# Performance work log

Hardware: AMD Instinct MI355X
Metric: run time of the kernel (lower is better)

Reference implementation:

```python
import jax, jax.numpy as jnp
import numpy as np

# ---- Clifford algebra Cl(4,1) setup -------------------------------------
SIG = [1, 1, 1, 1, -1]
GA = 1 << len(SIG)  # 32
B, S, E, H = 2, 512, 256, 8
HD = E // H


def _cayley_sign(sig):
    """sign[a,b] such that e_a * e_b = sign[a,b] * e_(a XOR b)."""
    n = len(sig)
    G = 1 << n
    M = np.zeros((G, G), np.float32)
    for a in range(G):
        for b in range(G):
            # canonical reordering sign
            ss = 0
            aa = a >> 1
            while aa:
                ss += bin(aa & b).count('1')
                aa >>= 1
            s = -1.0 if (ss & 1) else 1.0
            # metric contraction on shared basis vectors
            common = a & b
            for i in range(n):
                if (common >> i) & 1:
                    s *= sig[i]
            M[a, b] = s
    return M

SIGN = _cayley_sign(SIG)          # [GA, GA]
SIG_DIAG = np.diag(SIGN).copy()   # blade square signs (metric diagonal)


def _manifold_norm(x):
    # normalize each multivector over its GA components
    return x / jnp.sqrt(jnp.sum(x * x, axis=-1, keepdims=True) + 1e-6)


def _geo_linear(x, w):
    """Clifford linear layer: out[...,o,l] = sum_{i,m,n: m^n=l} w[o,i,m] x[...,i,n] sign(m,n).
    x: [B,S,In,GA], w: [Out,In,GA]. Loop over 32 fixed blades (signed permutation + GEMM)."""
    G = x.shape[-1]
    out = 0.0
    for m in range(G):
        perm = np.arange(G) ^ m              # n = m ^ l
        coeff = jnp.asarray(SIGN[m, perm])   # sign(m, n)
        xs = x[..., perm] * coeff            # [B,S,In,GA]
        out = out + jnp.einsum('oi,bsil->bsol', w[:, :, m], xs)
    return out


def _versor_linear(x, w):
    return _manifold_norm(_geo_linear(x, w))


def _forward(x, mask, wq, wk, wv, wo, gamma):
    b, s = x.shape[0], x.shape[1]
    q = _versor_linear(x, wq).reshape(b, s, H, HD, GA).transpose(0, 2, 1, 3, 4)
    k = _versor_linear(x, wk).reshape(b, s, H, HD, GA).transpose(0, 2, 1, 3, 4)
    v = _versor_linear(x, wv).reshape(b, s, H, HD, GA).transpose(0, 2, 1, 3, 4)
    q_flat = q.reshape(b * H, s, HD, GA)
    k_flat = k.reshape(b * H, s, HD, GA)
    sig_diag = jnp.asarray(SIG_DIAG)
    q_sig = q_flat * sig_diag                      # metric-weighted query
    scalar_score = jnp.einsum('bidl,bjdl->bij', q_sig, k_flat)   # [BH,S,S]
    q_norm_sq = jnp.sum(q_flat ** 2, axis=(-1, -2))[:, :, None]  # [BH,S,1]
    k_norm_sq = jnp.sum(k_flat ** 2, axis=(-1, -2))[:, None, :]  # [BH,1,S]
    bivector_norm = jnp.sqrt(jax.nn.relu(q_norm_sq * k_norm_sq - scalar_score ** 2) + 1e-6)
    score = (scalar_score + gamma * bivector_norm) / np.float32(np.sqrt(HD))
    # triangle update (seq > 1)
    score = score + 0.1 * jnp.matmul(jax.nn.softmax(score, axis=-1), score)
    score = score.reshape(b, H, s, s)
    score = jnp.where(mask[:, None, None, :] == 0, jnp.float32(-1e9), score)
    attn_probs = jax.nn.softmax(score, axis=-1)
    out = jnp.einsum('bhij,bhjdl->bhidl', attn_probs, v)
    out = out.transpose(0, 2, 1, 3, 4).reshape(b, s, E, GA)
    return _versor_linear(out, wo)


def setup_inputs() -> dict:
    key = jax.random.key(0)
    ks = jax.random.split(key, 6)
    std = np.float32((2.0 / (E * GA)) ** 0.5)
    x = jax.random.normal(ks[0], (B, S, E, GA), dtype=jnp.float32)
    wq = jax.random.normal(ks[1], (E, E, GA), dtype=jnp.float32) * std
    wk = jax.random.normal(ks[2], (E, E, GA), dtype=jnp.float32) * std
    wv = jax.random.normal(ks[3], (E, E, GA), dtype=jnp.float32) * std
    wo = jax.random.normal(ks[4], (E, E, GA), dtype=jnp.float32) * std
    gamma = jnp.asarray(0.1, dtype=jnp.float32)
    mask = jnp.ones((B, S), dtype=jnp.int32)
    return {'x': x, 'wq': wq, 'wk': wk, 'wv': wv, 'wo': wo, 'gamma': gamma, 'mask': mask}


def reference(x, wq, wk, wv, wo, gamma, mask):
    return _forward(x, mask, wq, wk, wv, wo, gamma)
```

## Files before the change

kernel.cpp:

```cpp
#include <hip/hip_runtime.h>
#include <stdint.h>

typedef unsigned short u16;
typedef unsigned int u32;
typedef __attribute__((ext_vector_type(8))) __bf16 bf16x8;
typedef __attribute__((ext_vector_type(4))) float f32x4;

#define DEVINL __device__ __forceinline__

DEVINL float bf2f(u16 u){ union{u32 i; float f;} c; c.i = ((u32)u)<<16; return c.f; }
DEVINL u16 f2bf(float f){ union{float f; u32 i;} c; c.f=f; u32 u=c.i; return (u16)((u + 0x7fffu + ((u>>16)&1u))>>16); }
DEVINL u32 pack2(float a, float b){ return (u32)f2bf(a) | ((u32)f2bf(b)<<16); }

DEVINL int sign_neg(int a, int b){
  int s = __popc((a>>1)&b) + __popc((a>>2)&b) + __popc((a>>3)&b) + __popc((a>>4)&b) + ((a&b)>>4);
  return s & 1;
}

struct GTab { int col[32][4]; int ph[32][4]; };
constexpr GTab make_gtab(){
  GTab g{};
  int gc[5][4] = {}; int gp[5][4] = {};
  for (int r=0;r<4;r++){
    const int a=(r>>1)&1, b=r&1;
    gc[0][r]=r^2; gp[0][r]=0;
    gc[1][r]=r^2; gp[1][r]= a?1:3;
    gc[2][r]=r^1; gp[2][r]= a?2:0;
    gc[3][r]=r^1; gp[3][r]=((a?2:0)+(b?1:3))&3;
    gc[4][r]=r;   gp[4][r]=(3+(a?2:0)+(b?2:0))&3;
  }
  for (int I=0;I<32;I++){
    for (int r=0;r<4;r++){ g.col[I][r]=r; g.ph[I][r]=0; }
    for (int bit=0;bit<5;bit++) if ((I>>bit)&1){
      for (int r=0;r<4;r++){
        const int c = g.col[I][r];
        g.ph[I][r]  = (g.ph[I][r] + gp[bit][c]) & 3;
        g.col[I][r] = gc[bit][c];
      }
    }
  }
  return g;
}
constexpr GTab GT = make_gtab();

DEVINL void mv2mat(const float (&x)[32], float (&Mre)[4][4], float (&Mim)[4][4]){
  #pragma unroll
  for (int r=0;r<4;r++)
    #pragma unroll
    for (int c=0;c<4;c++){ Mre[r][c]=0.f; Mim[r][c]=0.f; }
  #pragma unroll
  for (int l=0;l<32;l++){
    #pragma unroll
    for (int r=0;r<4;r++){
      constexpr const GTab& G = GT;
      const int c = G.col[l][r], p = G.ph[l][r];
      if (p==0) Mre[r][c] += x[l];
      else if (p==1) Mim[r][c] += x[l];
      else if (p==2) Mre[r][c] -= x[l];
      else Mim[r][c] -= x[l];
    }
  }
}

DEVINL void mat2mv(const float (&v)[4][8], float (&x)[32]){
  #pragma unroll
  for (int l=0;l<32;l++){
    float s = 0.f;
    #pragma unroll
    for (int r=0;r<4;r++){
      constexpr const GTab& G = GT;
      const int c = G.col[l][r], p = G.ph[l][r];
      if (p==0) s += v[c][r];
      else if (p==1) s += v[c][4+r];
      else if (p==2) s -= v[c][r];
      else s -= v[c][4+r];
    }
    x[l] = 0.25f*s;
  }
}

DEVINL void gload_lds16(const void* g, void* l){
  __builtin_amdgcn_global_load_lds(
    (const __attribute__((address_space(1))) void*)g,
    (__attribute__((address_space(3))) void*)l, 16, 0, 0);
}

__global__ __launch_bounds__(256) void k_v2m(const float* __restrict__ x, u16* __restrict__ Am){
  const int bs = blockIdx.x, i = threadIdx.x;
  const float* xp = x + ((size_t)bs*256 + i)*32;
  float xv[32];
  #pragma unroll
  for (int q=0;q<8;q++){
    float4 v = *(const float4*)(xp + q*4);
    xv[q*4+0]=v.x; xv[q*4+1]=v.y; xv[q*4+2]=v.z; xv[q*4+3]=v.w;
  }
  float Mre[4][4], Mim[4][4];
  mv2mat(xv, Mre, Mim);
  #pragma unroll
  for (int c=0;c<4;c++){
    u32 w0 = pack2(Mre[0][c], Mre[1][c]);
    u32 w1 = pack2(Mre[2][c], Mre[3][c]);
    u32 w2 = pack2(Mim[0][c], Mim[1][c]);
    u32 w3 = pack2(Mim[2][c], Mim[3][c]);
    *(uint4*)(Am + ((size_t)(bs*4+c))*2048 + i*8) = make_uint4(w0,w1,w2,w3);
  }
}

__global__ __launch_bounds__(256) void k_w2m(const float* __restrict__ wq, const float* __restrict__ wk,
                                             const float* __restrict__ wv, const float* __restrict__ wo,
                                             u16* __restrict__ Bfo){
  const int bid = blockIdx.x, i = threadIdx.x;
  const int wsel = bid>>8, o = bid&255;
  const float* w = wsel==0?wq: wsel==1?wk: wsel==2?wv: wo;
  const float* wp = w + ((size_t)o*256 + i)*32;
  float wv32[32];
  #pragma unroll
  for (int q=0;q<8;q++){
    float4 v = *(const float4*)(wp + q*4);
    wv32[q*4+0]=v.x; wv32[q*4+1]=v.y; wv32[q*4+2]=v.z; wv32[q*4+3]=v.w;
  }
  float Wre[4][4], Wim[4][4];
  mv2mat(wv32, Wre, Wim);
  u16* base = Bfo + (size_t)wsel*4194304 + (size_t)(i>>3)*131072 + (o>>1)*1024
            + ((i>>2)&1)*512;
  const int lanebase = (o&1)*8 + (i&3)*16;
  #pragma unroll
  for (int r8=0;r8<8;r8++){
    float e0,e1,e2,e3,e4,e5,e6,e7;
    if (r8<4){
      e0=Wre[r8][0]; e1=Wre[r8][1]; e2=Wre[r8][2]; e3=Wre[r8][3];
      e4=-Wim[r8][0]; e5=-Wim[r8][1]; e6=-Wim[r8][2]; e7=-Wim[r8][3];
    } else {
      e0=Wim[r8-4][0]; e1=Wim[r8-4][1]; e2=Wim[r8-4][2]; e3=Wim[r8-4][3];
      e4=Wre[r8-4][0]; e5=Wre[r8-4][1]; e6=Wre[r8-4][2]; e7=Wre[r8-4][3];
    }
    *(uint4*)(base + (lanebase + r8)*8) =
      make_uint4(pack2(e0,e1), pack2(e2,e3), pack2(e4,e5), pack2(e6,e7));
  }
}

DEVINL void mg_phase(int kq, int cbuf, const u16* __restrict__ Wsel, const int (&boff)[4][2],
                     const u16* __restrict__ Am, int row0, int sbase, int lane,
                     u16* SM, uint4 (&B0)[4], uint4 (&B0n)[4],
                     f32x4 (&acc)[4][4], int wm, int wn, int lo, int hi){
  const u16* Wq = Wsel + (size_t)kq*131072;
  uint4 B1[4];
  #pragma unroll
  for (int fn=0; fn<4; ++fn) B1[fn] = *(const uint4*)(Wq + boff[fn][1]);
  asm volatile("s_waitcnt vmcnt(8)" ::: "memory");
  __builtin_amdgcn_sched_barrier(0);
  __builtin_amdgcn_s_barrier();
  __builtin_amdgcn_sched_barrier(0);
  if (kq+1 < 32){
    #pragma unroll
    for (int cc=0;cc<4;cc++){
      const int base = sbase + cc*64;
      const int idx = base + lane;
      const int rr = idx>>3, g = idx&7;
      gload_lds16(Am + (size_t)(row0+rr)*2048 + (kq+1)*64 + ((g^(rr&7))*8),
                  SM + (cbuf^1)*8192 + base*8);
    }
  }
  const u16* Ab = SM + cbuf*8192;
  bf16x8 af0[4];
  #pragma unroll
  for (int f=0;f<4;f++){
    const int ra = wm*64 + f*16 + lo;
    af0[f] = *(const bf16x8*)(Ab + ra*64 + ((hi ^ (ra&7))*8));
  }
  if (kq+1 < 32){
    const u16* Wn = Wq + 131072;
    #pragma unroll
    for (int fn=0; fn<4; ++fn) B0n[fn] = *(const uint4*)(Wn + boff[fn][0]);
  }
  __builtin_amdgcn_s_setprio(1);
  #pragma unroll
  for (int fm=0;fm<4;fm++){
    #pragma unroll
    for (int fn=0;fn<4;fn++)
      acc[fm][fn] = __builtin_amdgcn_mfma_f32_16x16x32_bf16(
          af0[fm], *(const bf16x8*)&B0[fn], acc[fm][fn], 0,0,0);
  }
  __builtin_amdgcn_s_setprio(0);
  bf16x8 af1[4];
  #pragma unroll
  for (int f=0;f<4;f++){
    const int ra = wm*64 + f*16 + lo;
    af1[f] = *(const bf16x8*)(Ab + ra*64 + (((4+hi) ^ (ra&7))*8));
  }
  __builtin_amdgcn_s_setprio(1);
  #pragma unroll
  for (int fm=0;fm<4;fm++){
    #pragma unroll
    for (int fn=0;fn<4;fn++)
      acc[fm][fn] = __builtin_amdgcn_mfma_f32_16x16x32_bf16(
          af1[fm], *(const bf16x8*)&B1[fn], acc[fm][fn], 0,0,0);
  }
  __builtin_amdgcn_s_setprio(0);
}

template<int EPI>
__global__ __launch_bounds__(256) void k_mgemm(const u16* __restrict__ Am, const u16* __restrict__ Bfo,
                                               u16* __restrict__ qkv, float* __restrict__ dout,
                                               float* __restrict__ Nqp, float* __restrict__ Nkp){
  constexpr int NT = (EPI==0)?48:16;
  constexpr int NWG = 32*NT;
  __shared__ __align__(16) u16 SM[128*136];
  const int wg = blockIdx.x;
  const int bid = (wg&7)*(NWG/8) + (wg>>3);
  const int tn = bid>>5, tm = bid&31;
  const int row0 = tm*128, col0 = tn*128;
  const int sel   = (EPI==0)? (col0>>11) : 3;
  const int ncol0 = (EPI==0)? (col0&2047) : col0;
  const u16* Wsel = Bfo + (size_t)sel*4194304;
  const int t = threadIdx.x, lane = t&63, wid = t>>6;
  const int wm = wid>>1, wn = wid&1, lo = lane&15, hi = lane>>4;

  int boff[4][2];
  #pragma unroll
  for (int fn=0; fn<4; ++fn){
    const int nblk = (ncol0>>4) + wn*4 + fn;
    #pragma unroll
    for (int kk=0; kk<2; ++kk)
      boff[fn][kk] = (nblk*2+kk)*512 + lane*8;
  }

  f32x4 acc[4][4];
  #pragma unroll
  for(int a=0;a<4;a++){
    #pragma unroll
    for(int b=0;b<4;b++){ acc[a][b] = (f32x4){0.f,0.f,0.f,0.f}; }
  }

  const int sbase = (wid*4)*64;
  #pragma unroll
  for (int cc=0;cc<4;cc++){
    const int base = sbase + cc*64;
    const int idx = base + lane;
    const int rr = idx>>3, g = idx&7;
    gload_lds16(Am + (size_t)(row0+rr)*2048 + ((g^(rr&7))*8), SM + base*8);
  }
  uint4 B0a[4], B0b[4];
  #pragma unroll
  for (int fn=0; fn<4; ++fn) B0a[fn] = *(const uint4*)(Wsel + boff[fn][0]);

  #pragma unroll 1
  for (int kq2=0; kq2<16; ++kq2){
    mg_phase(2*kq2,   0, Wsel, boff, Am, row0, sbase, lane, SM, B0a, B0b, acc, wm, wn, lo, hi);
    mg_phase(2*kq2+1, 1, Wsel, boff, Am, row0, sbase, lane, SM, B0b, B0a, acc, wm, wn, lo, hi);
  }

  __syncthreads();
  #pragma unroll
  for (int fm=0;fm<4;fm++){
    #pragma unroll
    for (int r=0;r<4;r++){
      const int mL = wm*64 + fm*16 + hi*4 + r;
      #pragma unroll
      for (int fn=0;fn<4;fn++){
        const int nL = wn*64 + fn*16 + lo;
        SM[mL*136 + nL] = f2bf(acc[fm][fn][r]);
      }
    }
  }
  __syncthreads();
  const int bsL = t>>3, oLp = t&7;
  const int bs = (row0>>2) + bsL;
  const int o0w = ncol0>>3;
  float nsum = 0.f;
  #pragma unroll
  for (int u=0;u<2;u++){
    const int oL = oLp + u*8;
    float v[4][8];
    #pragma unroll
    for (int c=0;c<4;c++){
      uint4 q4 = *(const uint4*)(SM + (bsL*4+c)*136 + oL*8);
      v[c][0]=bf2f((u16)(q4.x&0xffffu)); v[c][1]=bf2f((u16)(q4.x>>16));
      v[c][2]=bf2f((u16)(q4.y&0xffffu)); v[c][3]=bf2f((u16)(q4.y>>16));
      v[c][4]=bf2f((u16)(q4.z&0xffffu)); v[c][5]=bf2f((u16)(q4.z>>16));
      v[c][6]=bf2f((u16)(q4.w&0xffffu)); v[c][7]=bf2f((u16)(q4.w>>16));
    }
    float xs[32];
    mat2mv(v, xs);
    float s = 0.f;
    #pragma unroll
    for (int l=0;l<32;l++) s += xs[l]*xs[l];
    const float rs = rsqrtf(s + 1e-6f);
    if constexpr (EPI==0){
      nsum += s/(s+1e-6f);
      if (sel == 0){
        #pragma unroll
        for (int l=0;l<32;l++) xs[l] = sign_neg(l,l)? -xs[l]*rs : xs[l]*rs;
      } else {
        #pragma unroll
        for (int l=0;l<32;l++) xs[l] *= rs;
      }
      u16* dst = qkv + ((size_t)bs*768 + sel*256 + o0w + oL)*32;
      #pragma unroll
      for (int q=0;q<4;q++)
        *(uint4*)(dst + q*8) = make_uint4(pack2(xs[q*8+0],xs[q*8+1]), pack2(xs[q*8+2],xs[q*8+3]),
                                          pack2(xs[q*8+4],xs[q*8+5]), pack2(xs[q*8+6],xs[q*8+7]));
    } else {
      float* dst = dout + ((size_t)bs*256 + o0w + oL)*32;
      #pragma unroll
      for (int q=0;q<8;q++)
        *(float4*)(dst + q*4) = make_float4(xs[q*4+0]*rs, xs[q*4+1]*rs, xs[q*4+2]*rs, xs[q*4+3]*rs);
    }
  }
  if constexpr (EPI==0){
    if (sel < 2){
      nsum += __shfl_xor(nsum,1); nsum += __shfl_xor(nsum,2); nsum += __shfl_xor(nsum,4);
      if ((t&7)==0){
        const int half = (o0w>>4)&1, h = o0w>>5;
        const int b = bs>>9, s_ = bs&511;
        float* nd = (sel==0)? Nqp : Nkp;
        nd[half*8192 + (b*8+h)*512 + s_] = nsum;
      }
    }
  }
}

DEVINL void mm_steps(const u16* Abase, int Astride, const u16* Bbase, int Bstride, int ksteps,
                     u16* Al, u16* Bl, f32x4 (&acc)[4][4], int lane, int wid){
  const int wm = wid>>1, wn = wid&1, lo = lane&15, hi = lane>>4;
  for (int s=0; s<ksteps; ++s){
    const int k0 = s*64;
    #pragma unroll
    for (int c=0;c<4;c++){
      const int gb = (wid*4+c)*64;
      const int idx = gb + lane;
      const int r = idx>>3, j = idx&7;
      const int sw = ((j^(r&7))*8);
      gload_lds16(Abase + (size_t)r*Astride + k0 + sw, Al + gb*8);
      gload_lds16(Bbase + (size_t)r*Bstride + k0 + sw, Bl + gb*8);
    }
    __syncthreads();
    #pragma unroll
    for (int kk=0; kk<2; ++kk){
      bf16x8 af[4], bfr[4];
      #pragma unroll
      for (int f=0;f<4;f++){
        const int ra = wm*64 + f*16 + lo;
        const int jc = kk*4 + hi;
        af[f] = *(const bf16x8*)(Al + ra*64 + ((jc^(ra&7))*8));
        const int rb = wn*64 + f*16 + lo;
        bfr[f] = *(const bf16x8*)(Bl + rb*64 + ((jc^(rb&7))*8));
      }
      #pragma unroll
      for (int fm=0;fm<4;fm++){
        #pragma unroll
        for (int fn=0;fn<4;fn++)
          acc[fm][fn] = __builtin_amdgcn_mfma_f32_16x16x32_bf16(af[fm], bfr[fn], acc[fm][fn], 0,0,0);
      }
    }
    __syncthreads();
  }
}

__global__ __launch_bounds__(256) void k_score(const u16* __restrict__ qkv, const float* __restrict__ Nqp,
                                               const float* __restrict__ Nkp, const float* __restrict__ gptr,
                                               float* __restrict__ S1, u16* __restrict__ S1T){
  __shared__ __align__(16) u16 Al[128*64];
  __shared__ __align__(16) u16 Bl[128*64];
  __shared__ __align__(16) u16 Tl[128*136];
  const int wg = blockIdx.x;
  const int bid = (wg&7)*32 + (wg>>3);
  const int bh = bid>>4, ti=(bid>>2)&3, tj=bid&3;
  const int b = bh>>3, h = bh&7;
  const int i0=ti*128, j0=tj*128;
  const int t=threadIdx.x, lane=t&63, wid=t>>6;
  const int wm=wid>>1, wn=wid&1, lo=lane&15, hi=lane>>4;
  f32x4 acc[4][4];
  #pragma unroll
  for(int a=0;a<4;a++){
    #pragma unroll
    for(int c=0;c<4;c++){ acc[a][c] = (f32x4){0.f,0.f,0.f,0.f}; }
  }
  const u16* Abase = qkv + ((size_t)(b*512+i0))*24576 + h*1024;
  const u16* Bbase = qkv + ((size_t)(b*512+j0))*24576 + 8192 + h*1024;
  mm_steps(Abase, 24576, Bbase, 24576, 16, Al, Bl, acc, lane, wid);
  const float gamma = *gptr;
  const float rhd = 0.17677669529663687f;
  float nkv[4];
  #pragma unroll
  for (int fn=0;fn<4;fn++){
    const int idx = bh*512 + j0 + wn*64 + fn*16 + lo;
    nkv[fn] = Nkp[idx] + Nkp[8192 + idx];
  }
  #pragma unroll
  for (int fm=0;fm<4;fm++){
    #pragma unroll
    for (int r=0;r<4;r++){
      const int iL = wm*64 + fm*16 + hi*4 + r;
      const int qidx = bh*512 + i0 + iL;
      const float nq = Nqp[qidx] + Nqp[8192 + qidx];
      #pragma unroll
      for (int fn=0;fn<4;fn++){
        const int jL = wn*64 + fn*16 + lo;
        const float ss = acc[fm][fn][r];
        const float biv = sqrtf(fmaxf(nq*nkv[fn] - ss*ss, 0.f) + 1e-6f);
        const float sc = (ss + gamma*biv)*rhd;
        S1[((size_t)bh*512 + i0 + iL)*512 + j0 + jL] = sc;
        Tl[jL*136 + iL] = f2bf(sc);
      }
    }
  }
  __syncthreads();
  const int jj = t>>1, half = t&1;
  u16* dst = S1T + ((size_t)bh*512 + (j0+jj))*512 + i0 + half*64;
  #pragma unroll
  for (int q=0;q<8;q++)
    *(uint4*)(dst + q*8) = *(const uint4*)(Tl + jj*136 + half*64 + q*8);
}

__global__ __launch_bounds__(256) void k_softmax(const float* __restrict__ S, const int* __restrict__ mask,
                                                 u16* __restrict__ P, int masked){
  const int t = threadIdx.x, lane = t&63, wid = t>>6;
  const int row = blockIdx.x*4 + wid;
  const int b = row>>12;
  const float* sp = S + (size_t)row*512;
  float4 a = *(const float4*)(sp + lane*4);
  float4 c = *(const float4*)(sp + 256 + lane*4);
  if (masked){
    const int* mp = mask + b*512;
    int4 ma = *(const int4*)(mp + lane*4);
    int4 mc = *(const int4*)(mp + 256 + lane*4);
    if (ma.x==0) a.x=-1e9f; if (ma.y==0) a.y=-1e9f; if (ma.z==0) a.z=-1e9f; if (ma.w==0) a.w=-1e9f;
    if (mc.x==0) c.x=-1e9f; if (mc.y==0) c.y=-1e9f; if (mc.z==0) c.z=-1e9f; if (mc.w==0) c.w=-1e9f;
  }
  float mx = fmaxf(fmaxf(fmaxf(a.x,a.y),fmaxf(a.z,a.w)), fmaxf(fmaxf(c.x,c.y),fmaxf(c.z,c.w)));
  #pragma unroll
  for (int o=1;o<64;o<<=1) mx = fmaxf(mx, __shfl_xor(mx,o));
  const float e0=__expf(a.x-mx), e1=__expf(a.y-mx), e2=__expf(a.z-mx), e3=__expf(a.w-mx);
  const float e4=__expf(c.x-mx), e5=__expf(c.y-mx), e6=__expf(c.z-mx), e7=__expf(c.w-mx);
  float sm = (e0+e1)+(e2+e3)+(e4+e5)+(e6+e7);
  #pragma unroll
  for (int o=1;o<64;o<<=1) sm += __shfl_xor(sm,o);
  const float inv = 1.f/sm;
  u16* pp = P + (size_t)row*512;
  *(uint2*)(pp + lane*4)       = make_uint2(pack2(e0*inv,e1*inv), pack2(e2*inv,e3*inv));
  *(uint2*)(pp + 256 + lane*4) = make_uint2(pack2(e4*inv,e5*inv), pack2(e6*inv,e7*inv));
}

__global__ __launch_bounds__(256) void k_tri(const u16* __restrict__ P1, const u16* __restrict__ S1T,
                                             float* __restrict__ S1){
  __shared__ __align__(16) u16 Al[128*64];
  __shared__ __align__(16) u16 Bl[128*64];
  const int wg = blockIdx.x;
  const int bid = (wg&7)*32 + (wg>>3);
  const int bh = bid>>4, ti=(bid>>2)&3, tj=bid&3;
  const int i0=ti*128, j0=tj*128;
  const int t=threadIdx.x, lane=t&63, wid=t>>6;
  const int wm=wid>>1, wn=wid&1, lo=lane&15, hi=lane>>4;
  f32x4 acc[4][4];
  #pragma unroll
  for(int a=0;a<4;a++){
    #pragma unroll
    for(int c=0;c<4;c++){ acc[a][c] = (f32x4){0.f,0.f,0.f,0.f}; }
  }
  const u16* Abase = P1  + ((size_t)bh*512 + i0)*512;
  const u16* Bbase = S1T + ((size_t)bh*512 + j0)*512;
  mm_steps(Abase, 512, Bbase, 512, 8, Al, Bl, acc, lane, wid);
  #pragma unroll
  for (int fm=0;fm<4;fm++){
    #pragma unroll
    for (int r=0;r<4;r++){
      const int iL = wm*64 + fm*16 + hi*4 + r;
      #pragma unroll
      for (int fn=0;fn<4;fn++){
        const int jL = wn*64 + fn*16 + lo;
        const size_t idx = ((size_t)bh*512 + i0 + iL)*512 + j0 + jL;
        S1[idx] = S1[idx] + 0.1f*acc[fm][fn][r];
      }
    }
  }
}

__global__ __launch_bounds__(256) void k_tr_v(const u16* __restrict__ qkv, u16* __restrict__ VT){
  __shared__ u16 tile[128*129];
  const int bid=blockIdx.x;
  const int bh = bid>>5, dch=(bid>>2)&7, sch=bid&3;
  const int b=bh>>3, h=bh&7;
  const int d0=dch*128, s0=sch*128;
  const int t=threadIdx.x;
  {
    const int r=t>>1, half=t&1;
    const u16* src = qkv + ((size_t)(b*512+s0+r))*24576 + 16384 + h*1024 + d0 + half*64;
    #pragma unroll
    for (int q=0;q<8;q++){
      uint4 v = *(const uint4*)(src + q*8);
      u16* dp = tile + r*129 + half*64 + q*8;
      dp[0]=(u16)(v.x&0xffffu); dp[1]=(u16)(v.x>>16); dp[2]=(u16)(v.y&0xffffu); dp[3]=(u16)(v.y>>16);
      dp[4]=(u16)(v.z&0xffffu); dp[5]=(u16)(v.z>>16); dp[6]=(u16)(v.w&0xffffu); dp[7]=(u16)(v.w>>16);
    }
  }
  __syncthreads();
  {
    const int rr=t>>1, half=t&1;
    u16* dst = VT + ((size_t)bh*1024 + d0+rr)*512 + s0 + half*64;
    #pragma unroll
    for (int q=0;q<4;q++){
      u32 w[8];
      #pragma unroll
      for (int e=0;e<8;e++){
        const int s = half*64 + q*16 + e*2;
        w[e] = (u32)tile[s*129+rr] | ((u32)tile[(s+1)*129+rr]<<16);
      }
      *(uint4*)(dst + q*16)     = make_uint4(w[0],w[1],w[2],w[3]);
      *(uint4*)(dst + q*16 + 8) = make_uint4(w[4],w[5],w[6],w[7]);
    }
  }
}

__global__ __launch_bounds__(256) void k_pv(const u16* __restrict__ P2, const u16* __restrict__ VT,
                                            u16* __restrict__ Am2){
  __shared__ __align__(16) u16 Al[128*64];
  __shared__ __align__(16) u16 Bl[128*64];
  __shared__ __align__(16) u16 Tl[128*136];
  const int wg = blockIdx.x;
  const int bid = (wg&7)*64 + (wg>>3);
  const int bh = bid>>5, ti=(bid>>3)&3, td=bid&7;
  const int b=bh>>3, h=bh&7;
  const int i0=ti*128, d0=td*128;
  const int t=threadIdx.x, lane=t&63, wid=t>>6;
  const int wm=wid>>1, wn=wid&1, lo=lane&15, hi=lane>>4;
  f32x4 acc[4][4];
  #pragma unroll
  for(int a=0;a<4;a++){
    #pragma unroll
    for(int c=0;c<4;c++){ acc[a][c] = (f32x4){0.f,0.f,0.f,0.f}; }
  }
  const u16* Abase = P2 + ((size_t)bh*512 + i0)*512;
  const u16* Bbase = VT + ((size_t)bh*1024 + d0)*512;
  mm_steps(Abase, 512, Bbase, 512, 8, Al, Bl, acc, lane, wid);
  #pragma unroll
  for (int fm=0;fm<4;fm++){
    #pragma unroll
    for (int r=0;r<4;r++){
      const int sL = wm*64 + fm*16 + hi*4 + r;
      #pragma unroll
      for (int fn=0;fn<4;fn++){
        const int dL = wn*64 + fn*16 + lo;
        Tl[sL*136 + dL] = f2bf(acc[fm][fn][r]);
      }
    }
  }
  __syncthreads();
  #pragma unroll
  for (int u=0;u<2;u++){
    const int idx = t + u*256;
    const int sL = idx>>2, hdL = idx&3;
    const u16* tp = Tl + sL*136 + hdL*32;
    float xv[32];
    #pragma unroll
    for (int q=0;q<4;q++){
      uint4 v = *(const uint4*)(tp + q*8);
      xv[q*8+0]=bf2f((u16)(v.x&0xffffu)); xv[q*8+1]=bf2f((u16)(v.x>>16));
      xv[q*8+2]=bf2f((u16)(v.y&0xffffu)); xv[q*8+3]=bf2f((u16)(v.y>>16));
      xv[q*8+4]=bf2f((u16)(v.z&0xffffu)); xv[q*8+5]=bf2f((u16)(v.z>>16));
      xv[q*8+6]=bf2f((u16)(v.w&0xffffu)); xv[q*8+7]=bf2f((u16)(v.w>>16));
    }
    float Mre[4][4], Mim[4][4];
    mv2mat(xv, Mre, Mim);
    const int e = h*32 + td*4 + hdL;
    const size_t mrow = ((size_t)(b*512 + i0 + sL))*4;
    #pragma unroll
    for (int c=0;c<4;c++){
      u32 w0 = pack2(Mre[0][c], Mre[1][c]);
      u32 w1 = pack2(Mre[2][c], Mre[3][c]);
      u32 w2 = pack2(Mim[0][c], Mim[1][c]);
      u32 w3 = pack2(Mim[2][c], Mim[3][c]);
      *(uint4*)(Am2 + (mrow + c)*2048 + e*8) = make_uint4(w0,w1,w2,w3);
    }
  }
}

extern "C" void kernel_launch(void* const* d_in, const int* in_sizes, int n_in,
                              void* d_out, int out_size, void* d_ws, size_t ws_size,
                              hipStream_t stream) {
  const float* x  = (const float*)d_in[0];
  const float* wq = (const float*)d_in[1];
  const float* wk = (const float*)d_in[2];
  const float* wv = (const float*)d_in[3];
  const float* wo = (const float*)d_in[4];
  const float* gamma = (const float*)d_in[5];
  const int*   mask  = (const int*)d_in[6];
  float* out = (float*)d_out;

  char* ws = (char*)d_ws;
  size_t off = 0;
  auto alloc = [&](size_t n){ char* p = ws + off; off += (n + 255) & ~(size_t)255; return p; };
  u16*  Am  = (u16*) alloc(16777216);
  u16*  Bfo = (u16*) alloc(33554432);
  u16*  qkv = (u16*) alloc(50331648);
  float* Nqp = (float*)alloc(65536);
  float* Nkp = (float*)alloc(65536);
  float* S1 = (float*)alloc(16777216);
  u16*  S1T = (u16*) alloc(8388608);
  u16*  P2  = (u16*) alloc(8388608);
  u16*  P1  = (u16*)Am;
  u16*  VT  = (u16*)S1;
  u16*  Am2 = (u16*)Am;

  k_v2m<<<1024, 256, 0, stream>>>(x, Am);
  k_w2m<<<1024, 256, 0, stream>>>(wq, wk, wv, wo, Bfo);
  k_mgemm<0><<<1536, 256, 0, stream>>>(Am, Bfo, qkv, nullptr, Nqp, Nkp);
  k_score<<<256, 256, 0, stream>>>(qkv, Nqp, Nkp, gamma, S1, S1T);
  k_softmax<<<2048, 256, 0, stream>>>(S1, mask, P1, 0);
  k_tri<<<256, 256, 0, stream>>>(P1, S1T, S1);
  k_softmax<<<2048, 256, 0, stream>>>(S1, mask, P2, 1);
  k_tr_v<<<512, 256, 0, stream>>>(qkv, VT);
  k_pv<<<512, 256, 0, stream>>>(P2, VT, Am2);
  k_mgemm<1><<<512, 256, 0, stream>>>(Am2, Bfo, nullptr, out, nullptr, nullptr);
}
```

Measured before the change: 275.6 us.

## Double-buffer LDS tiles in attention GEMMs to overlap global loads with MFMA

Replaces the single-buffered load-sync-compute loop used by the score, triangle and PV GEMM kernels with a ping-pong LDS scheme. The next K-tile's async global-to-LDS loads are issued right after the barrier and before the current tile's MFMAs, so memory latency can hide behind compute, and one barrier per step is removed. It also raises wave priority around the MFMA block and aliases the epilogue transpose buffer onto the GEMM buffers with an added barrier. LDS use goes up to 64KB per block in k_tri, which may reduce occupancy.

```diff
diff --git a/kernel.cpp b/kernel.cpp
--- a/kernel.cpp
+++ b/kernel.cpp
@@ -320,21 +320,38 @@
   }
 }
 
-DEVINL void mm_steps(const u16* Abase, int Astride, const u16* Bbase, int Bstride, int ksteps,
-                     u16* Al, u16* Bl, f32x4 (&acc)[4][4], int lane, int wid){
+DEVINL void mm_steps_p(const u16* Abase, int Astride, const u16* Bbase, int Bstride, int ksteps,
+                       u16* SM, f32x4 (&acc)[4][4], int lane, int wid){
   const int wm = wid>>1, wn = wid&1, lo = lane&15, hi = lane>>4;
+  #pragma unroll
+  for (int c=0;c<4;c++){
+    const int gb = (wid*4+c)*64;
+    const int idx = gb + lane;
+    const int r = idx>>3, j = idx&7;
+    const int sw = ((j^(r&7))*8);
+    gload_lds16(Abase + (size_t)r*Astride + sw, SM + gb*8);
+    gload_lds16(Bbase + (size_t)r*Bstride + sw, SM + 16384 + gb*8);
+  }
+  int cbuf = 0;
   for (int s=0; s<ksteps; ++s){
-    const int k0 = s*64;
-    #pragma unroll
-    for (int c=0;c<4;c++){
-      const int gb = (wid*4+c)*64;
-      const int idx = gb + lane;
-      const int r = idx>>3, j = idx&7;
-      const int sw = ((j^(r&7))*8);
-      gload_lds16(Abase + (size_t)r*Astride + k0 + sw, Al + gb*8);
-      gload_lds16(Bbase + (size_t)r*Bstride + k0 + sw, Bl + gb*8);
-    }
-    __syncthreads();
+    asm volatile("s_waitcnt vmcnt(0)" ::: "memory");
+    __builtin_amdgcn_sched_barrier(0);
+    __builtin_amdgcn_s_barrier();
+    __builtin_amdgcn_sched_barrier(0);
+    if (s+1 < ksteps){
+      const int k0 = (s+1)*64;
+      #pragma unroll
+      for (int c=0;c<4;c++){
+        const int gb = (wid*4+c)*64;
+        const int idx = gb + lane;
+        const int r = idx>>3, j = idx&7;
+        const int sw = ((j^(r&7))*8);
+        gload_lds16(Abase + (size_t)r*Astride + k0 + sw, SM + (cbuf^1)*8192 + gb*8);
+        gload_lds16(Bbase + (size_t)r*Bstride + k0 + sw, SM + 16384 + (cbuf^1)*8192 + gb*8);
+      }
+    }
+    const u16* Al = SM + cbuf*8192;
+    const u16* Blc = SM + 16384 + cbuf*8192;
     #pragma unroll
     for (int kk=0; kk<2; ++kk){
       bf16x8 af[4], bfr[4];
@@ -344,25 +361,26 @@
         const int jc = kk*4 + hi;
         af[f] = *(const bf16x8*)(Al + ra*64 + ((jc^(ra&7))*8));
         const int rb = wn*64 + f*16 + lo;
-        bfr[f] = *(const bf16x8*)(Bl + rb*64 + ((jc^(rb&7))*8));
-      }
+        bfr[f] = *(const bf16x8*)(Blc + rb*64 + ((jc^(rb&7))*8));
+      }
+      __builtin_amdgcn_s_setprio(1);
       #pragma unroll
       for (int fm=0;fm<4;fm++){
         #pragma unroll
         for (int fn=0;fn<4;fn++)
           acc[fm][fn] = __builtin_amdgcn_mfma_f32_16x16x32_bf16(af[fm], bfr[fn], acc[fm][fn], 0,0,0);
       }
-    }
-    __syncthreads();
+      __builtin_amdgcn_s_setprio(0);
+    }
+    cbuf ^= 1;
   }
 }
 
 __global__ __launch_bounds__(256) void k_score(const u16* __restrict__ qkv, const float* __restrict__ Nqp,
                                                const float* __restrict__ Nkp, const float* __restrict__ gptr,
                                                float* __restrict__ S1, u16* __restrict__ S1T){
-  __shared__ __align__(16) u16 Al[128*64];
-  __shared__ __align__(16) u16 Bl[128*64];
-  __shared__ __align__(16) u16 Tl[128*136];
+  __shared__ __align__(16) u16 SM[32768];
+  u16* Tl = SM;
   const int wg = blockIdx.x;
   const int bid = (wg&7)*32 + (wg>>3);
   const int bh = bid>>4, ti=(bid>>2)&3, tj=bid&3;
@@ -378,7 +396,8 @@
   }
   const u16* Abase = qkv + ((size_t)(b*512+i0))*24576 + h*1024;
   const u16* Bbase = qkv + ((size_t)(b*512+j0))*24576 + 8192 + h*1024;
-  mm_steps(Abase, 24576, Bbase, 24576, 16, Al, Bl, acc, lane, wid);
+  mm_steps_p(Abase, 24576, Bbase, 24576, 16, SM, acc, lane, wid);
+  __syncthreads();
   const float gamma = *gptr;
   const float rhd = 0.17677669529663687f;
   float nkv[4];
@@ -444,8 +463,7 @@
 
 __global__ __launch_bounds__(256) void k_tri(const u16* __restrict__ P1, const u16* __restrict__ S1T,
                                              float* __restrict__ S1){
-  __shared__ __align__(16) u16 Al[128*64];
-  __shared__ __align__(16) u16 Bl[128*64];
+  __shared__ __align__(16) u16 SM[32768];
   const int wg = blockIdx.x;
   const int bid = (wg&7)*32 + (wg>>3);
   const int bh = bid>>4, ti=(bid>>2)&3, tj=bid&3;
@@ -460,7 +478,7 @@
   }
   const u16* Abase = P1  + ((size_t)bh*512 + i0)*512;
   const u16* Bbase = S1T + ((size_t)bh*512 + j0)*512;
-  mm_steps(Abase, 512, Bbase, 512, 8, Al, Bl, acc, lane, wid);
+  mm_steps_p(Abase, 512, Bbase, 512, 8, SM, acc, lane, wid);
   #pragma unroll
   for (int fm=0;fm<4;fm++){
     #pragma unroll
@@ -514,9 +532,8 @@
 
 __global__ __launch_bounds__(256) void k_pv(const u16* __restrict__ P2, const u16* __restrict__ VT,
                                             u16* __restrict__ Am2){
-  __shared__ __align__(16) u16 Al[128*64];
-  __shared__ __align__(16) u16 Bl[128*64];
-  __shared__ __align__(16) u16 Tl[128*136];
+  __shared__ __align__(16) u16 SM[32768];
+  u16* Tl = SM;
   const int wg = blockIdx.x;
   const int bid = (wg&7)*64 + (wg>>3);
   const int bh = bid>>5, ti=(bid>>3)&3, td=bid&7;
@@ -532,7 +549,8 @@
   }
   const u16* Abase = P2 + ((size_t)bh*512 + i0)*512;
   const u16* Bbase = VT + ((size_t)bh*1024 + d0)*512;
-  mm_steps(Abase, 512, Bbase, 512, 8, Al, Bl, acc, lane, wid);
+  mm_steps_p(Abase, 512, Bbase, 512, 8, SM, acc, lane, wid);
+  __syncthreads();
   #pragma unroll
   for (int fm=0;fm<4;fm++){
     #pragma unroll
```

Result: faster. 264.0 us (median of 2 runs) (-4.2%).
